# Performance work log

Hardware: AMD Instinct MI355X
Metric: run time of the kernel (lower is better)

Reference implementation:

```python
import jax, jax.numpy as jnp
import numpy as np

TAU = 1.0
NUM_CENTROIDS = 8
COMMITMENT_COST = 0.25


def setup_inputs() -> dict:
    key = jax.random.key(0)
    kx, kc = jax.random.split(key)
    B, T, D = 8, 2048, 512
    K = 4096  # codebook_size
    x = jax.random.normal(kx, (B, T, D), dtype=jnp.float32)
    # variance_scaling(1.0, fan_in, uniform): limit = sqrt(3/D)
    limit = np.sqrt(3.0 / D).astype(np.float32)
    codebook = jax.random.uniform(kc, (K, D), dtype=jnp.float32, minval=-limit, maxval=limit)
    return {"x": x, "codebook": codebook}


def _squared_euclidean_distance(a, b):
    # a: [N, D], b: [K, D] -> [N, K]
    a2 = jnp.sum(a * a, axis=-1, keepdims=True)          # [N, 1]
    b2 = jnp.sum(b * b, axis=-1)                          # [K]
    ab = a @ b.T                                          # [N, K]
    return a2 - 2.0 * ab + b2


def reference(x, codebook):
    B, T, D = x.shape
    K = codebook.shape[0]
    flat = x.reshape(-1, D)
    distances = _squared_euclidean_distance(flat, codebook).reshape(B, T, K)
    weights = jax.nn.softmax(-distances / TAU, axis=-1)
    top_weights, top_indices = jax.lax.top_k(weights, NUM_CENTROIDS)  # [B,T,k]
    top_weights = top_weights / jnp.sum(top_weights, axis=-1, keepdims=True)
    # decode_ids: weighted sum of gathered codebook rows (== one-hot einsum)
    gathered = jnp.take(codebook, top_indices, axis=0)                # [B,T,k,D]
    quantized = jnp.einsum('btk,btkd->btd', top_weights, gathered)
    # train=True losses (entropy_loss_ratio == 0 -> skipped)
    e_latent_loss = jnp.mean((jax.lax.stop_gradient(quantized) - x) ** 2) * COMMITMENT_COST
    q_latent_loss = jnp.mean((quantized - jax.lax.stop_gradient(x)) ** 2)
    loss = e_latent_loss.astype(jnp.float32) + q_latent_loss.astype(jnp.float32)
    # straight-through estimator
    quantized = x + jax.lax.stop_gradient(quantized - x)
    return quantized, loss
```

## Files before the change

kernel.cpp:

```cpp
#include <hip/hip_runtime.h>
#include <stdint.h>

#define D_DIM 512
#define K_CB  4096
#define N_TOK 16384
#define TOPK  8

#define TOKB  64
#define NPASS 8
#define NSEL  16

typedef __attribute__((ext_vector_type(4)))  int    i32x4;
typedef __attribute__((ext_vector_type(8)))  int    i32x8;
typedef __attribute__((ext_vector_type(16))) float  f32x16;
typedef __attribute__((ext_vector_type(4)))  float  f32x4;

template<int N>
__device__ __forceinline__ void inskey(unsigned int k, unsigned int (&ts)[N]) {
    #pragma unroll
    for (int q = 0; q < N; ++q) {
        unsigned int hi = ts[q] > k ? ts[q] : k;
        unsigned int lo = ts[q] > k ? k : ts[q];
        ts[q] = hi; k = lo;
    }
}

__global__ __launch_bounds__(256) void conv_cb_kernel(
    const float* __restrict__ cb, unsigned char* __restrict__ cbf8,
    float* __restrict__ cnorm, float* __restrict__ loss,
    unsigned int* __restrict__ ticket) {
    const int t = threadIdx.x, g = blockIdx.x;
    if (g == 0 && t == 0) { *loss = 0.f; *ticket = 0u; }
    const int r = t >> 3, s = t & 7;
    const float* src = cb + ((size_t)(g * 32 + r)) * D_DIM + s * 64;
    float sq = 0.f;
    unsigned int d[16];
    #pragma unroll
    for (int i = 0; i < 16; ++i) {
        float4 v = ((const float4*)src)[i];
        sq += v.x*v.x + v.y*v.y + v.z*v.z + v.w*v.w;
        int dd = __builtin_amdgcn_cvt_pk_fp8_f32(64.f * v.x, 64.f * v.y, 0, false);
        dd     = __builtin_amdgcn_cvt_pk_fp8_f32(64.f * v.z, 64.f * v.w, dd, true);
        d[i] = (unsigned int)dd;
    }
    sq += __shfl_down(sq, 4, 8);
    sq += __shfl_down(sq, 2, 8);
    sq += __shfl_down(sq, 1, 8);
    if (s == 0) cnorm[g * 32 + r] = sq;
    unsigned char* dst = cbf8 + (size_t)g * 16384 + (size_t)s * 2048;
    i32x4 w0 = {(int)d[0],  (int)d[1],  (int)d[2],  (int)d[3]};
    i32x4 w1 = {(int)d[4],  (int)d[5],  (int)d[6],  (int)d[7]};
    i32x4 w2 = {(int)d[8],  (int)d[9],  (int)d[10], (int)d[11]};
    i32x4 w3 = {(int)d[12], (int)d[13], (int)d[14], (int)d[15]};
    *(i32x4*)(dst +        (size_t)r * 16)        = w0;
    *(i32x4*)(dst + 1024 + (size_t)r * 16)        = w1;
    *(i32x4*)(dst +        (size_t)(32 + r) * 16) = w2;
    *(i32x4*)(dst + 1024 + (size_t)(32 + r) * 16) = w3;
}

__global__ __launch_bounds__(1024) void vq_fused(
    const float* __restrict__ x, const float* __restrict__ cb,
    const unsigned char* __restrict__ cbf8, const float* __restrict__ cnorm,
    float* __restrict__ out, float* __restrict__ loss_acc,
    unsigned int* __restrict__ ticket)
{
    __shared__ union {
        unsigned char xs8[TOKB * D_DIM];
        unsigned int  keys[256 * 64];
    } u;
    __shared__ float ncn[K_CB];
    __shared__ unsigned int pk[64 * 64];
    __shared__ int   tki[TOKB * NSEL];
    __shared__ float tks[TOKB * NSEL];
    __shared__ float tkw[TOKB * TOPK];
    __shared__ int   tkif[TOKB * TOPK];
    __shared__ float redbuf[16];

    const int t    = threadIdx.x;
    const int lane = t & 63;
    const int w    = t >> 6;
    const int m32  = lane & 31;
    const int half = lane >> 5;
    const int tok0 = blockIdx.x * TOKB;

    {
        const int token = t >> 4, c = t & 15;
        const int s2 = c >> 1, lh = c & 1;
        const f32x4* src = (const f32x4*)(x + (size_t)(tok0 + token) * D_DIM + c * 32);
        unsigned int d[8];
        #pragma unroll
        for (int i = 0; i < 8; ++i) {
            f32x4 v = src[i];
            int dd = __builtin_amdgcn_cvt_pk_fp8_f32(16.f * v.x, 16.f * v.y, 0, false);
            dd     = __builtin_amdgcn_cvt_pk_fp8_f32(16.f * v.z, 16.f * v.w, dd, true);
            d[i] = (unsigned int)dd;
        }
        const int lf = lh * 32 + (token & 31);
        unsigned char* base = u.xs8 + (token >> 5) * 16384 + s2 * 2048 + lf * 16;
        i32x4 lo = {(int)d[0], (int)d[1], (int)d[2], (int)d[3]};
        i32x4 hi = {(int)d[4], (int)d[5], (int)d[6], (int)d[7]};
        *(i32x4*)(base)        = lo;
        *(i32x4*)(base + 1024) = hi;
    }
    {
        float4 v = ((const float4*)cnorm)[t];
        float4 nv = {32768.f - 512.f * v.x, 32768.f - 512.f * v.y,
                     32768.f - 512.f * v.z, 32768.f - 512.f * v.w};
        *(float4*)&ncn[t * 4] = nv;
    }
    __syncthreads();

    unsigned int ts0[8], ts1[8];
    #pragma unroll
    for (int i = 0; i < 8; ++i) { ts0[i] = 0u; ts1[i] = 0u; }

    const char* ab0 = (const char*)cbf8 + (size_t)w * 16384 + (size_t)lane * 16;
    const unsigned char* pb = u.xs8 + lane * 16;

    for (int pp = 0; pp < NPASS; ++pp) {
        const int p  = (pp + w) & 7;
        const int ga = p * 16 + w;
        f32x16 a0, a1;
        #pragma unroll
        for (int g = 0; g < 4; ++g) {
            float4 n0 = *(const float4*)&ncn[ga * 32 + g * 8 + 4 * half];
            a0[g*4+0]=n0.x; a0[g*4+1]=n0.y; a0[g*4+2]=n0.z; a0[g*4+3]=n0.w;
            a1[g*4+0]=n0.x; a1[g*4+1]=n0.y; a1[g*4+2]=n0.z; a1[g*4+3]=n0.w;
        }
        const char* ab = ab0 + (size_t)p * 262144;
        __builtin_amdgcn_s_setprio(1);
        #pragma unroll 2
        for (int s = 0; s < 8; ++s) {
            i32x4 al = *(const i32x4*)(ab + s * 2048);
            i32x4 ah = *(const i32x4*)(ab + s * 2048 + 1024);
            i32x4 bl0 = *(const i32x4*)(pb + s * 2048);
            i32x4 bh0 = *(const i32x4*)(pb + s * 2048 + 1024);
            i32x4 bl1 = *(const i32x4*)(pb + s * 2048 + 16384);
            i32x4 bh1 = *(const i32x4*)(pb + s * 2048 + 17408);
            i32x8 A  = __builtin_shufflevector(al,  ah,  0,1,2,3,4,5,6,7);
            i32x8 B0 = __builtin_shufflevector(bl0, bh0, 0,1,2,3,4,5,6,7);
            i32x8 B1 = __builtin_shufflevector(bl1, bh1, 0,1,2,3,4,5,6,7);
            a0 = __builtin_amdgcn_mfma_scale_f32_32x32x64_f8f6f4(
                     A, B0, a0, 0, 0, 0, 0x7F7F7F7F, 0, 0x7F7F7F7F);
            a1 = __builtin_amdgcn_mfma_scale_f32_32x32x64_f8f6f4(
                     A, B1, a1, 0, 0, 0, 0x7F7F7F7F, 0, 0x7F7F7F7F);
        }
        __builtin_amdgcn_s_setprio(0);
        const unsigned int K0 = 4095u - (unsigned int)(ga * 32) - 4u * (unsigned int)half;
        #pragma unroll
        for (int r = 0; r < 16; ++r) {
            const unsigned int cr = (unsigned int)((r & 3) + 8 * (r >> 2));
            inskey((__float_as_uint(a0[r]) & 0xFFFFF000u) | (K0 - cr), ts0);
            inskey((__float_as_uint(a1[r]) & 0xFFFFF000u) | (K0 - cr), ts1);
        }
    }

    __syncthreads();
    {
        const int kk = (w * 2 + half) * 8;
        #pragma unroll
        for (int e = 0; e < 8; ++e) {
            u.keys[(kk + e) * 64 + m32]      = ts0[e];
            u.keys[(kk + e) * 64 + 32 + m32] = ts1[e];
        }
    }
    __syncthreads();
    if (t < 256) {
        const int token = t >> 2, sub = t & 3;
        unsigned int bs[16];
        #pragma unroll
        for (int i = 0; i < 16; ++i) bs[i] = 0u;
        #pragma unroll 2
        for (int k = 0; k < 64; ++k) inskey(u.keys[(sub * 64 + k) * 64 + token], bs);
        #pragma unroll
        for (int e = 0; e < 16; ++e) pk[token * 64 + sub * 16 + e] = bs[e];
    }
    __syncthreads();
    if (t < TOKB) {
        unsigned int bs[NSEL];
        #pragma unroll
        for (int i = 0; i < NSEL; ++i) bs[i] = 0u;
        #pragma unroll 2
        for (int k = 0; k < 64; ++k) inskey(pk[t * 64 + k], bs);
        #pragma unroll
        for (int r = 0; r < NSEL; ++r) tki[t * NSEL + r] = 4095 - (int)(bs[r] & 0xFFFu);
    }
    __syncthreads();
    {
        const int token = t >> 4, sl = t & 15;
        const f32x4* xr = (const f32x4*)(x + (size_t)(tok0 + token) * D_DIM);
        f32x4 xv[8];
        #pragma unroll
        for (int i = 0; i < 8; ++i) xv[i] = xr[sl + 16 * i];
        #pragma unroll
        for (int hh = 0; hh < 2; ++hh) {
            float pd[8];
            #pragma unroll
            for (int e = 0; e < 8; ++e) {
                const int idx = tki[token * NSEL + hh * 8 + e];
                const f32x4* cr = (const f32x4*)(cb + (size_t)idx * D_DIM);
                float dot = 0.f;
                #pragma unroll
                for (int i = 0; i < 8; ++i) {
                    f32x4 cv = cr[sl + 16 * i];
                    dot += xv[i].x*cv.x + xv[i].y*cv.y + xv[i].z*cv.z + xv[i].w*cv.w;
                }
                pd[e] = dot;
            }
            #pragma unroll
            for (int e = 0; e < 8; ++e) {
                pd[e] += __shfl_down(pd[e], 8, 16);
                pd[e] += __shfl_down(pd[e], 4, 16);
                pd[e] += __shfl_down(pd[e], 2, 16);
                pd[e] += __shfl_down(pd[e], 1, 16);
            }
            if (sl == 0) {
                #pragma unroll
                for (int e = 0; e < 8; ++e)
                    tks[token * NSEL + hh * 8 + e] =
                        2.f * pd[e] - cnorm[tki[token * NSEL + hh * 8 + e]];
            }
        }
    }
    __syncthreads();
    if (t < TOKB) {
        unsigned int bs[8];
        #pragma unroll
        for (int i = 0; i < 8; ++i) bs[i] = 0u;
        #pragma unroll
        for (int e = 0; e < NSEL; ++e) {
            unsigned int uu = __float_as_uint(tks[t * NSEL + e]);
            uu ^= (unsigned int)((int)uu >> 31) | 0x80000000u;
            inskey((uu & 0xFFFFFFF0u) | (unsigned int)e, bs);
        }
        const float m = tks[t * NSEL + (int)(bs[0] & 15u)];
        float wv[TOPK], sum = 0.f;
        int ids[TOPK];
        #pragma unroll
        for (int r = 0; r < TOPK; ++r) {
            const int e = (int)(bs[r] & 15u);
            wv[r] = __expf(tks[t * NSEL + e] - m); sum += wv[r];
            ids[r] = tki[t * NSEL + e];
        }
        const float inv = 1.f / sum;
        #pragma unroll
        for (int r = 0; r < TOPK; ++r) {
            tkw[t * TOPK + r] = wv[r] * inv;
            tkif[t * TOPK + r] = ids[r];
        }
    }
    __syncthreads();
    float lsum = 0.f;
    #pragma unroll 1
    for (int it = 0; it < (TOKB * (D_DIM / 4)) / 1024; ++it) {
        const int p = it * 1024 + t;
        const int token = p >> 7, d4 = p & 127;
        float4 q = {0.f, 0.f, 0.f, 0.f};
        #pragma unroll
        for (int e = 0; e < TOPK; ++e) {
            const float wv = tkw[token * TOPK + e];
            const int  idx = tkif[token * TOPK + e];
            const float4 cv = ((const float4*)cb)[(size_t)idx * (D_DIM / 4) + d4];
            q.x += wv * cv.x; q.y += wv * cv.y; q.z += wv * cv.z; q.w += wv * cv.w;
        }
        const size_t go = (size_t)(tok0 + token) * (D_DIM / 4) + d4;
        f32x4 xv = __builtin_nontemporal_load((const f32x4*)x + go);
        const float ex = q.x - xv.x, ey = q.y - xv.y, ez = q.z - xv.z, ew = q.w - xv.w;
        lsum += ex*ex + ey*ey + ez*ez + ew*ew;
        f32x4 qv = {q.x, q.y, q.z, q.w};
        __builtin_nontemporal_store(qv, (f32x4*)out + go);
    }
    #pragma unroll
    for (int off = 32; off > 0; off >>= 1) lsum += __shfl_down(lsum, off, 64);
    if (lane == 0) redbuf[w] = lsum;
    __syncthreads();
    if (t == 0) {
        float s = 0.f;
        #pragma unroll
        for (int i = 0; i < 16; ++i) s += redbuf[i];
        atomicAdd(loss_acc, s);
        __threadfence();
        unsigned int prev = atomicAdd(ticket, 1u);
        if (prev == (unsigned int)(gridDim.x - 1)) {
            __threadfence();
            float total = atomicAdd(loss_acc, 0.f);
            out[(size_t)N_TOK * D_DIM] = 1.25f * total / (float)((size_t)N_TOK * D_DIM);
        }
    }
}

extern "C" void kernel_launch(void* const* d_in, const int* in_sizes, int n_in,
                              void* d_out, int out_size, void* d_ws, size_t ws_size,
                              hipStream_t stream) {
    const float* x  = (const float*)d_in[0];
    const float* cb = (const float*)d_in[1];
    float* out = (float*)d_out;

    char* ws = (char*)d_ws;
    unsigned char* cbf8   = (unsigned char*)ws;
    float*         cnorm  = (float*)(ws + 2097152);
    float*         loss   = (float*)(ws + 2113536);
    unsigned int*  ticket = (unsigned int*)(ws + 2113600);

    conv_cb_kernel<<<128, 256, 0, stream>>>(cb, cbf8, cnorm, loss, ticket);
    vq_fused<<<N_TOK / TOKB, 1024, 0, stream>>>(x, cb, cbf8, cnorm, out, loss, ticket);
}
```

Baseline: 228.2 us.

## Halve token tile to 32 with 512-thread blocks and prefetch codebook fragments

Shrinks the per-block token tile from 64 to 32 and the block from 1024 to 512 threads, requesting 4 blocks per CU, so each wave computes one 32x32 accumulator per pass over 16 passes instead of two over 8. The first two K-slices of the next codebook tile are prefetched into registers during top-k insertion to hide global load latency. Shared-memory arrays are padded (stride 65/17) to avoid bank conflicts, and the codebook conversion kernel is rewritten for the new block mapping. Reuse of each codebook fragment across tokens halves, so global/L2 traffic for the fp8 codebook doubles, in exchange for more resident blocks and better latency hiding.

```diff
diff --git a/kernel.cpp b/kernel.cpp
--- a/kernel.cpp
+++ b/kernel.cpp
@@ -6,8 +6,8 @@
 #define N_TOK 16384
 #define TOPK  8
 
-#define TOKB  64
-#define NPASS 8
+#define TOKB  32
+#define NPASS 16
 #define NSEL  16
 
 typedef __attribute__((ext_vector_type(4)))  int    i32x4;
@@ -29,36 +29,37 @@
     const float* __restrict__ cb, unsigned char* __restrict__ cbf8,
     float* __restrict__ cnorm, float* __restrict__ loss,
     unsigned int* __restrict__ ticket) {
-    const int t = threadIdx.x, g = blockIdx.x;
-    if (g == 0 && t == 0) { *loss = 0.f; *ticket = 0u; }
-    const int r = t >> 3, s = t & 7;
-    const float* src = cb + ((size_t)(g * 32 + r)) * D_DIM + s * 64;
+    const int t = threadIdx.x, gb = blockIdx.x;
+    if (gb == 0 && t == 0) { *loss = 0.f; *ticket = 0u; }
+    const int r16 = t >> 4, c = t & 15;
+    const int row = gb * 16 + r16;
+    const float* src = cb + (size_t)row * D_DIM + c * 32;
     float sq = 0.f;
-    unsigned int d[16];
+    unsigned int d[8];
     #pragma unroll
-    for (int i = 0; i < 16; ++i) {
+    for (int i = 0; i < 8; ++i) {
         float4 v = ((const float4*)src)[i];
         sq += v.x*v.x + v.y*v.y + v.z*v.z + v.w*v.w;
         int dd = __builtin_amdgcn_cvt_pk_fp8_f32(64.f * v.x, 64.f * v.y, 0, false);
         dd     = __builtin_amdgcn_cvt_pk_fp8_f32(64.f * v.z, 64.f * v.w, dd, true);
         d[i] = (unsigned int)dd;
     }
-    sq += __shfl_down(sq, 4, 8);
-    sq += __shfl_down(sq, 2, 8);
-    sq += __shfl_down(sq, 1, 8);
-    if (s == 0) cnorm[g * 32 + r] = sq;
-    unsigned char* dst = cbf8 + (size_t)g * 16384 + (size_t)s * 2048;
-    i32x4 w0 = {(int)d[0],  (int)d[1],  (int)d[2],  (int)d[3]};
-    i32x4 w1 = {(int)d[4],  (int)d[5],  (int)d[6],  (int)d[7]};
-    i32x4 w2 = {(int)d[8],  (int)d[9],  (int)d[10], (int)d[11]};
-    i32x4 w3 = {(int)d[12], (int)d[13], (int)d[14], (int)d[15]};
-    *(i32x4*)(dst +        (size_t)r * 16)        = w0;
-    *(i32x4*)(dst + 1024 + (size_t)r * 16)        = w1;
-    *(i32x4*)(dst +        (size_t)(32 + r) * 16) = w2;
-    *(i32x4*)(dst + 1024 + (size_t)(32 + r) * 16) = w3;
+    sq += __shfl_down(sq, 8, 16);
+    sq += __shfl_down(sq, 4, 16);
+    sq += __shfl_down(sq, 2, 16);
+    sq += __shfl_down(sq, 1, 16);
+    if (c == 0) cnorm[row] = sq;
+    const int g = row >> 5, row32 = row & 31;
+    const int s = c >> 1, khalf = c & 1;
+    unsigned char* base = cbf8 + (size_t)g * 16384 + (size_t)s * 2048
+                        + (size_t)(khalf * 32 + row32) * 16;
+    i32x4 lo = {(int)d[0], (int)d[1], (int)d[2], (int)d[3]};
+    i32x4 hi = {(int)d[4], (int)d[5], (int)d[6], (int)d[7]};
+    *(i32x4*)(base)        = lo;
+    *(i32x4*)(base + 1024) = hi;
 }
 
-__global__ __launch_bounds__(1024) void vq_fused(
+__global__ __launch_bounds__(512, 4) void vq_fused(
     const float* __restrict__ x, const float* __restrict__ cb,
     const unsigned char* __restrict__ cbf8, const float* __restrict__ cnorm,
     float* __restrict__ out, float* __restrict__ loss_acc,
@@ -66,15 +67,15 @@
 {
     __shared__ union {
         unsigned char xs8[TOKB * D_DIM];
-        unsigned int  keys[256 * 64];
+        unsigned int  keys[256 * 32];
     } u;
     __shared__ float ncn[K_CB];
-    __shared__ unsigned int pk[64 * 64];
-    __shared__ int   tki[TOKB * NSEL];
-    __shared__ float tks[TOKB * NSEL];
+    __shared__ unsigned int pk[TOKB * 65];
+    __shared__ int   tki[TOKB * 17];
+    __shared__ float tks[TOKB * 17];
     __shared__ float tkw[TOKB * TOPK];
     __shared__ int   tkif[TOKB * TOPK];
-    __shared__ float redbuf[16];
+    __shared__ float redbuf[8];
 
     const int t    = threadIdx.x;
     const int lane = t & 63;
@@ -83,6 +84,18 @@
     const int half = lane >> 5;
     const int tok0 = blockIdx.x * TOKB;
 
+    const char* cb8l = (const char*)cbf8 + (size_t)lane * 16;
+
+    i32x4 pf0l, pf0h, pf1l, pf1h;
+    {
+        const int p0  = (2 * w) & 15;
+        const char* abp = cb8l + (size_t)(p0 * 8 + w) * 16384;
+        pf0l = *(const i32x4*)(abp);
+        pf0h = *(const i32x4*)(abp + 1024);
+        pf1l = *(const i32x4*)(abp + 2048);
+        pf1h = *(const i32x4*)(abp + 3072);
+    }
+
     {
         const int token = t >> 4, c = t & 15;
         const int s2 = c >> 1, lh = c & 1;
@@ -95,85 +108,110 @@
             dd     = __builtin_amdgcn_cvt_pk_fp8_f32(16.f * v.z, 16.f * v.w, dd, true);
             d[i] = (unsigned int)dd;
         }
-        const int lf = lh * 32 + (token & 31);
-        unsigned char* base = u.xs8 + (token >> 5) * 16384 + s2 * 2048 + lf * 16;
+        unsigned char* base = u.xs8 + s2 * 2048 + (lh * 32 + token) * 16;
         i32x4 lo = {(int)d[0], (int)d[1], (int)d[2], (int)d[3]};
         i32x4 hi = {(int)d[4], (int)d[5], (int)d[6], (int)d[7]};
         *(i32x4*)(base)        = lo;
         *(i32x4*)(base + 1024) = hi;
     }
     {
-        float4 v = ((const float4*)cnorm)[t];
-        float4 nv = {32768.f - 512.f * v.x, 32768.f - 512.f * v.y,
-                     32768.f - 512.f * v.z, 32768.f - 512.f * v.w};
-        *(float4*)&ncn[t * 4] = nv;
-    }
-    __syncthreads();
-
-    unsigned int ts0[8], ts1[8];
+        float4 v0 = ((const float4*)cnorm)[t];
+        float4 v1 = ((const float4*)cnorm)[t + 512];
+        float4 n0 = {32768.f - 512.f * v0.x, 32768.f - 512.f * v0.y,
+                     32768.f - 512.f * v0.z, 32768.f - 512.f * v0.w};
+        float4 n1 = {32768.f - 512.f * v1.x, 32768.f - 512.f * v1.y,
+                     32768.f - 512.f * v1.z, 32768.f - 512.f * v1.w};
+        *(float4*)&ncn[t * 4]         = n0;
+        *(float4*)&ncn[(t + 512) * 4] = n1;
+    }
+    __syncthreads();
+
+    unsigned int tsA[8], tsB[8];
     #pragma unroll
-    for (int i = 0; i < 8; ++i) { ts0[i] = 0u; ts1[i] = 0u; }
-
-    const char* ab0 = (const char*)cbf8 + (size_t)w * 16384 + (size_t)lane * 16;
+    for (int i = 0; i < 8; ++i) { tsA[i] = 0u; tsB[i] = 0u; }
+
     const unsigned char* pb = u.xs8 + lane * 16;
 
     for (int pp = 0; pp < NPASS; ++pp) {
-        const int p  = (pp + w) & 7;
-        const int ga = p * 16 + w;
-        f32x16 a0, a1;
+        const int p  = (pp + 2 * w) & 15;
+        const int ga = p * 8 + w;
+        f32x16 acc;
         #pragma unroll
         for (int g = 0; g < 4; ++g) {
             float4 n0 = *(const float4*)&ncn[ga * 32 + g * 8 + 4 * half];
-            a0[g*4+0]=n0.x; a0[g*4+1]=n0.y; a0[g*4+2]=n0.z; a0[g*4+3]=n0.w;
-            a1[g*4+0]=n0.x; a1[g*4+1]=n0.y; a1[g*4+2]=n0.z; a1[g*4+3]=n0.w;
-        }
-        const char* ab = ab0 + (size_t)p * 262144;
+            acc[g*4+0]=n0.x; acc[g*4+1]=n0.y; acc[g*4+2]=n0.z; acc[g*4+3]=n0.w;
+        }
+        const char* ab = cb8l + (size_t)ga * 16384;
         __builtin_amdgcn_s_setprio(1);
+        {
+            i32x4 bl0 = *(const i32x4*)(pb);
+            i32x4 bh0 = *(const i32x4*)(pb + 1024);
+            i32x8 A0 = __builtin_shufflevector(pf0l, pf0h, 0,1,2,3,4,5,6,7);
+            i32x8 B0 = __builtin_shufflevector(bl0, bh0, 0,1,2,3,4,5,6,7);
+            acc = __builtin_amdgcn_mfma_scale_f32_32x32x64_f8f6f4(
+                      A0, B0, acc, 0, 0, 0, 0x7F7F7F7F, 0, 0x7F7F7F7F);
+            i32x4 bl1 = *(const i32x4*)(pb + 2048);
+            i32x4 bh1 = *(const i32x4*)(pb + 3072);
+            i32x8 A1 = __builtin_shufflevector(pf1l, pf1h, 0,1,2,3,4,5,6,7);
+            i32x8 B1 = __builtin_shufflevector(bl1, bh1, 0,1,2,3,4,5,6,7);
+            acc = __builtin_amdgcn_mfma_scale_f32_32x32x64_f8f6f4(
+                      A1, B1, acc, 0, 0, 0, 0x7F7F7F7F, 0, 0x7F7F7F7F);
+        }
         #pragma unroll 2
-        for (int s = 0; s < 8; ++s) {
+        for (int s = 2; s < 8; ++s) {
             i32x4 al = *(const i32x4*)(ab + s * 2048);
             i32x4 ah = *(const i32x4*)(ab + s * 2048 + 1024);
-            i32x4 bl0 = *(const i32x4*)(pb + s * 2048);
-            i32x4 bh0 = *(const i32x4*)(pb + s * 2048 + 1024);
-            i32x4 bl1 = *(const i32x4*)(pb + s * 2048 + 16384);
-            i32x4 bh1 = *(const i32x4*)(pb + s * 2048 + 17408);
-            i32x8 A  = __builtin_shufflevector(al,  ah,  0,1,2,3,4,5,6,7);
-            i32x8 B0 = __builtin_shufflevector(bl0, bh0, 0,1,2,3,4,5,6,7);
-            i32x8 B1 = __builtin_shufflevector(bl1, bh1, 0,1,2,3,4,5,6,7);
-            a0 = __builtin_amdgcn_mfma_scale_f32_32x32x64_f8f6f4(
-                     A, B0, a0, 0, 0, 0, 0x7F7F7F7F, 0, 0x7F7F7F7F);
-            a1 = __builtin_amdgcn_mfma_scale_f32_32x32x64_f8f6f4(
-                     A, B1, a1, 0, 0, 0, 0x7F7F7F7F, 0, 0x7F7F7F7F);
+            i32x4 bl = *(const i32x4*)(pb + s * 2048);
+            i32x4 bh = *(const i32x4*)(pb + s * 2048 + 1024);
+            i32x8 A = __builtin_shufflevector(al, ah, 0,1,2,3,4,5,6,7);
+            i32x8 B = __builtin_shufflevector(bl, bh, 0,1,2,3,4,5,6,7);
+            acc = __builtin_amdgcn_mfma_scale_f32_32x32x64_f8f6f4(
+                      A, B, acc, 0, 0, 0, 0x7F7F7F7F, 0, 0x7F7F7F7F);
         }
         __builtin_amdgcn_s_setprio(0);
+        if (pp < NPASS - 1) {
+            const int p2 = (pp + 1 + 2 * w) & 15;
+            const char* abn = cb8l + (size_t)(p2 * 8 + w) * 16384;
+            pf0l = *(const i32x4*)(abn);
+            pf0h = *(const i32x4*)(abn + 1024);
+            pf1l = *(const i32x4*)(abn + 2048);
+            pf1h = *(const i32x4*)(abn + 3072);
+        }
         const unsigned int K0 = 4095u - (unsigned int)(ga * 32) - 4u * (unsigned int)half;
-        #pragma unroll
-        for (int r = 0; r < 16; ++r) {
-            const unsigned int cr = (unsigned int)((r & 3) + 8 * (r >> 2));
-            inskey((__float_as_uint(a0[r]) & 0xFFFFF000u) | (K0 - cr), ts0);
-            inskey((__float_as_uint(a1[r]) & 0xFFFFF000u) | (K0 - cr), ts1);
-        }
-    }
-
-    __syncthreads();
-    {
-        const int kk = (w * 2 + half) * 8;
+        if ((pp & 1) == 0) {
+            #pragma unroll
+            for (int r = 0; r < 16; ++r) {
+                const unsigned int cr = (unsigned int)((r & 3) + 8 * (r >> 2));
+                inskey((__float_as_uint(acc[r]) & 0xFFFFF000u) | (K0 - cr), tsA);
+            }
+        } else {
+            #pragma unroll
+            for (int r = 0; r < 16; ++r) {
+                const unsigned int cr = (unsigned int)((r & 3) + 8 * (r >> 2));
+                inskey((__float_as_uint(acc[r]) & 0xFFFFF000u) | (K0 - cr), tsB);
+            }
+        }
+    }
+
+    __syncthreads();
+    {
+        const int L0 = w * 4 + half * 2;
         #pragma unroll
         for (int e = 0; e < 8; ++e) {
-            u.keys[(kk + e) * 64 + m32]      = ts0[e];
-            u.keys[(kk + e) * 64 + 32 + m32] = ts1[e];
-        }
-    }
-    __syncthreads();
-    if (t < 256) {
+            u.keys[(L0 * 8 + e) * 32 + m32]       = tsA[e];
+            u.keys[((L0 + 1) * 8 + e) * 32 + m32] = tsB[e];
+        }
+    }
+    __syncthreads();
+    if (t < 128) {
         const int token = t >> 2, sub = t & 3;
         unsigned int bs[16];
         #pragma unroll
         for (int i = 0; i < 16; ++i) bs[i] = 0u;
         #pragma unroll 2
-        for (int k = 0; k < 64; ++k) inskey(u.keys[(sub * 64 + k) * 64 + token], bs);
-        #pragma unroll
-        for (int e = 0; e < 16; ++e) pk[token * 64 + sub * 16 + e] = bs[e];
+        for (int k = 0; k < 64; ++k) inskey(u.keys[(sub * 64 + k) * 32 + token], bs);
+        #pragma unroll
+        for (int e = 0; e < 16; ++e) pk[token * 65 + sub * 16 + e] = bs[e];
     }
     __syncthreads();
     if (t < TOKB) {
@@ -181,9 +219,9 @@
         #pragma unroll
         for (int i = 0; i < NSEL; ++i) bs[i] = 0u;
         #pragma unroll 2
-        for (int k = 0; k < 64; ++k) inskey(pk[t * 64 + k], bs);
-        #pragma unroll
-        for (int r = 0; r < NSEL; ++r) tki[t * NSEL + r] = 4095 - (int)(bs[r] & 0xFFFu);
+        for (int k = 0; k < 64; ++k) inskey(pk[t * 65 + k], bs);
+        #pragma unroll
+        for (int r = 0; r < NSEL; ++r) tki[t * 17 + r] = 4095 - (int)(bs[r] & 0xFFFu);
     }
     __syncthreads();
     {
@@ -197,7 +235,7 @@
             float pd[8];
             #pragma unroll
             for (int e = 0; e < 8; ++e) {
-                const int idx = tki[token * NSEL + hh * 8 + e];
+                const int idx = tki[token * 17 + hh * 8 + e];
                 const f32x4* cr = (const f32x4*)(cb + (size_t)idx * D_DIM);
                 float dot = 0.f;
                 #pragma unroll
@@ -217,8 +255,8 @@
             if (sl == 0) {
                 #pragma unroll
                 for (int e = 0; e < 8; ++e)
-                    tks[token * NSEL + hh * 8 + e] =
-                        2.f * pd[e] - cnorm[tki[token * NSEL + hh * 8 + e]];
+                    tks[token * 17 + hh * 8 + e] =
+                        2.f * pd[e] - cnorm[tki[token * 17 + hh * 8 + e]];
             }
         }
     }
@@ -229,18 +267,18 @@
         for (int i = 0; i < 8; ++i) bs[i] = 0u;
         #pragma unroll
         for (int e = 0; e < NSEL; ++e) {
-            unsigned int uu = __float_as_uint(tks[t * NSEL + e]);
+            unsigned int uu = __float_as_uint(tks[t * 17 + e]);
             uu ^= (unsigned int)((int)uu >> 31) | 0x80000000u;
             inskey((uu & 0xFFFFFFF0u) | (unsigned int)e, bs);
         }
-        const float m = tks[t * NSEL + (int)(bs[0] & 15u)];
+        const float m = tks[t * 17 + (int)(bs[0] & 15u)];
         float wv[TOPK], sum = 0.f;
         int ids[TOPK];
         #pragma unroll
         for (int r = 0; r < TOPK; ++r) {
             const int e = (int)(bs[r] & 15u);
-            wv[r] = __expf(tks[t * NSEL + e] - m); sum += wv[r];
-            ids[r] = tki[t * NSEL + e];
+            wv[r] = __expf(tks[t * 17 + e] - m); sum += wv[r];
+            ids[r] = tki[t * 17 + e];
         }
         const float inv = 1.f / sum;
         #pragma unroll
@@ -252,8 +290,8 @@
     __syncthreads();
     float lsum = 0.f;
     #pragma unroll 1
-    for (int it = 0; it < (TOKB * (D_DIM / 4)) / 1024; ++it) {
-        const int p = it * 1024 + t;
+    for (int it = 0; it < (TOKB * (D_DIM / 4)) / 512; ++it) {
+        const int p = it * 512 + t;
         const int token = p >> 7, d4 = p & 127;
         float4 q = {0.f, 0.f, 0.f, 0.f};
         #pragma unroll
@@ -277,7 +315,7 @@
     if (t == 0) {
         float s = 0.f;
         #pragma unroll
-        for (int i = 0; i < 16; ++i) s += redbuf[i];
+        for (int i = 0; i < 8; ++i) s += redbuf[i];
         atomicAdd(loss_acc, s);
         __threadfence();
         unsigned int prev = atomicAdd(ticket, 1u);
@@ -302,6 +340,6 @@
     float*         loss   = (float*)(ws + 2113536);
     unsigned int*  ticket = (unsigned int*)(ws + 2113600);
 
-    conv_cb_kernel<<<128, 256, 0, stream>>>(cb, cbf8, cnorm, loss, ticket);
-    vq_fused<<<N_TOK / TOKB, 1024, 0, stream>>>(x, cb, cbf8, cnorm, out, loss, ticket);
+    conv_cb_kernel<<<256, 256, 0, stream>>>(cb, cbf8, cnorm, loss, ticket);
+    vq_fused<<<N_TOK / TOKB, 512, 0, stream>>>(x, cb, cbf8, cnorm, out, loss, ticket);
 }
```

Result: no change. 231.2 us (+1.3%).
